# Kernel optimization log

Hardware: AMD Instinct MI355X
Metric: run time of the kernel (lower is better)

The kernel has to match this reference:

```python
import jax, jax.numpy as jnp
import numpy as np

EDGE_DIM = 64
NODE_DIM = 128
N_EDGES = 1_600_000
N_NODES = 50_000
LN_EPS = 1e-5


def setup_inputs() -> dict:
    key = jax.random.key(0)
    k1, k2, k3, k4 = jax.random.split(key, 4)
    edge_attr = jax.random.normal(k1, (N_EDGES, EDGE_DIM), dtype=jnp.float32)
    edge_index = jax.random.randint(k2, (2, N_EDGES), 0, N_NODES, dtype=jnp.int64)
    # Linear(edge_feat_dim, node_feat_dim) params (Kaiming-uniform-ish init)
    bound = 1.0 / np.sqrt(EDGE_DIM)
    W = jax.random.uniform(k3, (EDGE_DIM, NODE_DIM), dtype=jnp.float32, minval=-bound, maxval=bound)
    b = jax.random.uniform(k4, (NODE_DIM,), dtype=jnp.float32, minval=-bound, maxval=bound)
    gamma = jnp.ones((NODE_DIM,), dtype=jnp.float32)
    beta = jnp.zeros((NODE_DIM,), dtype=jnp.float32)
    return {"edge_attr": edge_attr, "W": W, "b": b, "gamma": gamma, "beta": beta,
            "edge_index": edge_index, "num_nodes": N_NODES}


def reference(edge_attr, W, b, gamma, beta, edge_index, num_nodes):
    # Edge transform: Linear -> ReLU -> LayerNorm
    h = jax.nn.relu(edge_attr @ W + b)  # [E, node_dim]
    mu = jnp.mean(h, axis=-1, keepdims=True)
    var = jnp.mean((h - mu) ** 2, axis=-1, keepdims=True)
    h = (h - mu) * jax.lax.rsqrt(var + LN_EPS) * gamma + beta
    src, dst = edge_index[0], edge_index[1]
    # Dual-endpoint scatter-add of transformed edge features
    node_features = (jax.ops.segment_sum(h, dst, num_segments=num_nodes)
                     + jax.ops.segment_sum(h, src, num_segments=num_nodes))  # [N, node_dim]
    ones = jnp.ones(src.shape[0], dtype=h.dtype)
    degree = (jax.ops.segment_sum(ones, src, num_segments=num_nodes)
              + jax.ops.segment_sum(ones, dst, num_segments=num_nodes))  # [N]
    degree = jnp.clip(degree, 1.0)[:, None]
    return node_features / degree
```

## Files before the change

### kernel.cpp

```cpp
#include <hip/hip_runtime.h>

constexpr int ED = 64;
constexpr int ND = 128;

__global__ __launch_bounds__(256)
void edge_scatter_kernel(const float* __restrict__ x,
                         const float* __restrict__ W,
                         const float* __restrict__ bias,
                         const float* __restrict__ gamma,
                         const float* __restrict__ beta,
                         const int*   __restrict__ ei,
                         int E,
                         float* __restrict__ out,
                         float* __restrict__ deg)
{
    __shared__ float4 Wq[32 * 64];

    for (int t = threadIdx.x; t < 32 * 64; t += 256) {
        const int k2 = t >> 6, j = t & 63;
        const float* Wr = W + (size_t)(2 * k2) * ND;
        Wq[t] = make_float4(Wr[j], Wr[64 + j], Wr[ND + j], Wr[ND + 64 + j]);
    }
    __syncthreads();

    const int lane = threadIdx.x & 63;
    const int wid  = blockIdx.x * (blockDim.x >> 6) + (threadIdx.x >> 6);
    const int nw   = gridDim.x * (blockDim.x >> 6);

    const float b0 = bias[lane],  b1 = bias[lane + 64];
    const float g0 = gamma[lane], g1 = gamma[lane + 64];
    const float p0 = beta[lane],  p1 = beta[lane + 64];

    const int ngroups = E >> 2;
    const int4* x4 = (const int4*)x;

    for (int g = wid; g < ngroups; g += nw) {
        const int e0 = g << 2;

        const int4 xi = x4[(size_t)g * 64 + lane];

        float h00 = b0, h01 = b1, h10 = b0, h11 = b1;
        float h20 = b0, h21 = b1, h30 = b0, h31 = b1;

#pragma unroll
        for (int kq = 0; kq < 16; ++kq) {
            const float4 wA = Wq[(2 * kq) * 64 + lane];
            const float4 wB = Wq[(2 * kq + 1) * 64 + lane];

            {
                const int ls = 0 * 16 + kq;
                const float a0 = __int_as_float(__builtin_amdgcn_readlane(xi.x, ls));
                const float a1 = __int_as_float(__builtin_amdgcn_readlane(xi.y, ls));
                const float a2 = __int_as_float(__builtin_amdgcn_readlane(xi.z, ls));
                const float a3 = __int_as_float(__builtin_amdgcn_readlane(xi.w, ls));
                h00 = fmaf(a0, wA.x, h00); h01 = fmaf(a0, wA.y, h01);
                h00 = fmaf(a1, wA.z, h00); h01 = fmaf(a1, wA.w, h01);
                h00 = fmaf(a2, wB.x, h00); h01 = fmaf(a2, wB.y, h01);
                h00 = fmaf(a3, wB.z, h00); h01 = fmaf(a3, wB.w, h01);
            }
            {
                const int ls = 1 * 16 + kq;
                const float a0 = __int_as_float(__builtin_amdgcn_readlane(xi.x, ls));
                const float a1 = __int_as_float(__builtin_amdgcn_readlane(xi.y, ls));
                const float a2 = __int_as_float(__builtin_amdgcn_readlane(xi.z, ls));
                const float a3 = __int_as_float(__builtin_amdgcn_readlane(xi.w, ls));
                h10 = fmaf(a0, wA.x, h10); h11 = fmaf(a0, wA.y, h11);
                h10 = fmaf(a1, wA.z, h10); h11 = fmaf(a1, wA.w, h11);
                h10 = fmaf(a2, wB.x, h10); h11 = fmaf(a2, wB.y, h11);
                h10 = fmaf(a3, wB.z, h10); h11 = fmaf(a3, wB.w, h11);
            }
            {
                const int ls = 2 * 16 + kq;
                const float a0 = __int_as_float(__builtin_amdgcn_readlane(xi.x, ls));
                const float a1 = __int_as_float(__builtin_amdgcn_readlane(xi.y, ls));
                const float a2 = __int_as_float(__builtin_amdgcn_readlane(xi.z, ls));
                const float a3 = __int_as_float(__builtin_amdgcn_readlane(xi.w, ls));
                h20 = fmaf(a0, wA.x, h20); h21 = fmaf(a0, wA.y, h21);
                h20 = fmaf(a1, wA.z, h20); h21 = fmaf(a1, wA.w, h21);
                h20 = fmaf(a2, wB.x, h20); h21 = fmaf(a2, wB.y, h21);
                h20 = fmaf(a3, wB.z, h20); h21 = fmaf(a3, wB.w, h21);
            }
            {
                const int ls = 3 * 16 + kq;
                const float a0 = __int_as_float(__builtin_amdgcn_readlane(xi.x, ls));
                const float a1 = __int_as_float(__builtin_amdgcn_readlane(xi.y, ls));
                const float a2 = __int_as_float(__builtin_amdgcn_readlane(xi.z, ls));
                const float a3 = __int_as_float(__builtin_amdgcn_readlane(xi.w, ls));
                h30 = fmaf(a0, wA.x, h30); h31 = fmaf(a0, wA.y, h31);
                h30 = fmaf(a1, wA.z, h30); h31 = fmaf(a1, wA.w, h31);
                h30 = fmaf(a2, wB.x, h30); h31 = fmaf(a2, wB.y, h31);
                h30 = fmaf(a3, wB.z, h30); h31 = fmaf(a3, wB.w, h31);
            }
        }

        h00 = fmaxf(h00, 0.f); h01 = fmaxf(h01, 0.f);
        h10 = fmaxf(h10, 0.f); h11 = fmaxf(h11, 0.f);
        h20 = fmaxf(h20, 0.f); h21 = fmaxf(h21, 0.f);
        h30 = fmaxf(h30, 0.f); h31 = fmaxf(h31, 0.f);

        float s0 = h00 + h01, q0 = fmaf(h00, h00, h01 * h01);
        float s1 = h10 + h11, q1 = fmaf(h10, h10, h11 * h11);
        float s2 = h20 + h21, q2 = fmaf(h20, h20, h21 * h21);
        float s3 = h30 + h31, q3 = fmaf(h30, h30, h31 * h31);
#pragma unroll
        for (int m = 1; m < 64; m <<= 1) {
            s0 += __shfl_xor(s0, m, 64); q0 += __shfl_xor(q0, m, 64);
            s1 += __shfl_xor(s1, m, 64); q1 += __shfl_xor(q1, m, 64);
            s2 += __shfl_xor(s2, m, 64); q2 += __shfl_xor(q2, m, 64);
            s3 += __shfl_xor(s3, m, 64); q3 += __shfl_xor(q3, m, 64);
        }
        const float inv = 1.0f / ND;
        const float mu0 = s0 * inv, rs0 = rsqrtf(q0 * inv - mu0 * mu0 + 1e-5f);
        const float mu1 = s1 * inv, rs1 = rsqrtf(q1 * inv - mu1 * mu1 + 1e-5f);
        const float mu2 = s2 * inv, rs2 = rsqrtf(q2 * inv - mu2 * mu2 + 1e-5f);
        const float mu3 = s3 * inv, rs3 = rsqrtf(q3 * inv - mu3 * mu3 + 1e-5f);

        const float y00 = (h00 - mu0) * rs0 * g0 + p0, y01 = (h01 - mu0) * rs0 * g1 + p1;
        const float y10 = (h10 - mu1) * rs1 * g0 + p0, y11 = (h11 - mu1) * rs1 * g1 + p1;
        const float y20 = (h20 - mu2) * rs2 * g0 + p0, y21 = (h21 - mu2) * rs2 * g1 + p1;
        const float y30 = (h30 - mu3) * rs3 * g0 + p0, y31 = (h31 - mu3) * rs3 * g1 + p1;

        const int sn0 = ei[e0 + 0], dn0 = ei[E + e0 + 0];
        const int sn1 = ei[e0 + 1], dn1 = ei[E + e0 + 1];
        const int sn2 = ei[e0 + 2], dn2 = ei[E + e0 + 2];
        const int sn3 = ei[e0 + 3], dn3 = ei[E + e0 + 3];

        unsafeAtomicAdd(&out[(size_t)dn0 * ND + lane],      y00);
        unsafeAtomicAdd(&out[(size_t)dn0 * ND + 64 + lane], y01);
        unsafeAtomicAdd(&out[(size_t)sn0 * ND + lane],      y00);
        unsafeAtomicAdd(&out[(size_t)sn0 * ND + 64 + lane], y01);
        unsafeAtomicAdd(&out[(size_t)dn1 * ND + lane],      y10);
        unsafeAtomicAdd(&out[(size_t)dn1 * ND + 64 + lane], y11);
        unsafeAtomicAdd(&out[(size_t)sn1 * ND + lane],      y10);
        unsafeAtomicAdd(&out[(size_t)sn1 * ND + 64 + lane], y11);
        unsafeAtomicAdd(&out[(size_t)dn2 * ND + lane],      y20);
        unsafeAtomicAdd(&out[(size_t)dn2 * ND + 64 + lane], y21);
        unsafeAtomicAdd(&out[(size_t)sn2 * ND + lane],      y20);
        unsafeAtomicAdd(&out[(size_t)sn2 * ND + 64 + lane], y21);
        unsafeAtomicAdd(&out[(size_t)dn3 * ND + lane],      y30);
        unsafeAtomicAdd(&out[(size_t)dn3 * ND + 64 + lane], y31);
        unsafeAtomicAdd(&out[(size_t)sn3 * ND + lane],      y30);
        unsafeAtomicAdd(&out[(size_t)sn3 * ND + 64 + lane], y31);

        int nid = dn0;
        if (lane == 1) nid = dn1;
        if (lane == 2) nid = dn2;
        if (lane == 3) nid = dn3;
        if (lane == 4) nid = sn0;
        if (lane == 5) nid = sn1;
        if (lane == 6) nid = sn2;
        if (lane == 7) nid = sn3;
        if (lane < 8) unsafeAtomicAdd(&deg[nid], 1.0f);
    }

    for (int e = (ngroups << 2) + wid; e < E; e += nw) {
        const int xv = __float_as_int(x[(size_t)e * ED + lane]);
        float h0 = b0, h1 = b1;
#pragma unroll
        for (int kq = 0; kq < 16; ++kq) {
            const float4 wA = Wq[(2 * kq) * 64 + lane];
            const float4 wB = Wq[(2 * kq + 1) * 64 + lane];
            const float a0 = __int_as_float(__builtin_amdgcn_readlane(xv, 4 * kq + 0));
            const float a1 = __int_as_float(__builtin_amdgcn_readlane(xv, 4 * kq + 1));
            const float a2 = __int_as_float(__builtin_amdgcn_readlane(xv, 4 * kq + 2));
            const float a3 = __int_as_float(__builtin_amdgcn_readlane(xv, 4 * kq + 3));
            h0 = fmaf(a0, wA.x, h0); h1 = fmaf(a0, wA.y, h1);
            h0 = fmaf(a1, wA.z, h0); h1 = fmaf(a1, wA.w, h1);
            h0 = fmaf(a2, wB.x, h0); h1 = fmaf(a2, wB.y, h1);
            h0 = fmaf(a3, wB.z, h0); h1 = fmaf(a3, wB.w, h1);
        }
        h0 = fmaxf(h0, 0.f); h1 = fmaxf(h1, 0.f);
        float s = h0 + h1, q = fmaf(h0, h0, h1 * h1);
#pragma unroll
        for (int m = 1; m < 64; m <<= 1) {
            s += __shfl_xor(s, m, 64); q += __shfl_xor(q, m, 64);
        }
        const float mu = s / ND, rs = rsqrtf(q / ND - mu * mu + 1e-5f);
        const float y0 = (h0 - mu) * rs * g0 + p0, y1 = (h1 - mu) * rs * g1 + p1;
        const int sn = ei[e], dn = ei[E + e];
        unsafeAtomicAdd(&out[(size_t)dn * ND + lane],      y0);
        unsafeAtomicAdd(&out[(size_t)dn * ND + 64 + lane], y1);
        unsafeAtomicAdd(&out[(size_t)sn * ND + lane],      y0);
        unsafeAtomicAdd(&out[(size_t)sn * ND + 64 + lane], y1);
        if (lane == 0) unsafeAtomicAdd(&deg[dn], 1.0f);
        if (lane == 1) unsafeAtomicAdd(&deg[sn], 1.0f);
    }
}

__global__ void finalize_kernel(float4* __restrict__ out,
                                const float* __restrict__ deg,
                                int n4)
{
    const int i = blockIdx.x * blockDim.x + threadIdx.x;
    if (i < n4) {
        const float d = fmaxf(deg[i >> 5], 1.0f);
        float4 v = out[i];
        v.x /= d; v.y /= d; v.z /= d; v.w /= d;
        out[i] = v;
    }
}

extern "C" void kernel_launch(void* const* d_in, const int* in_sizes, int n_in,
                              void* d_out, int out_size, void* d_ws, size_t ws_size,
                              hipStream_t stream)
{
    const float* x     = (const float*)d_in[0];
    const float* W     = (const float*)d_in[1];
    const float* bias  = (const float*)d_in[2];
    const float* gamma = (const float*)d_in[3];
    const float* beta  = (const float*)d_in[4];
    const int*   ei    = (const int*)d_in[5];

    const int E       = in_sizes[0] / ED;
    const int n_nodes = out_size / ND;

    float* out = (float*)d_out;
    float* deg = (float*)d_ws;

    hipMemsetAsync(d_out, 0, (size_t)out_size * sizeof(float), stream);
    hipMemsetAsync(d_ws,  0, (size_t)n_nodes * sizeof(float), stream);

    edge_scatter_kernel<<<4096, 256, 0, stream>>>(x, W, bias, gamma, beta,
                                                  ei, E, out, deg);

    finalize_kernel<<<(out_size / 4 + 255) / 256, 256, 0, stream>>>(
        (float4*)out, deg, out_size / 4);
}
```

Measured before the change: 1.898 ms.

## Replace atomic scatter-add with CSR build and per-node gather

Splits the fused kernel into stages. First, compute the LayerNorm-ed edge features into a workspace buffer while counting node degrees. Then prefix-scan the counts, fill a node-to-edge adjacency list, and have one wavefront per node gather and average its incident edge rows. This removes the per-element float atomics on the output, at the cost of a large intermediate write and read plus a single-block scan. It also adds nontemporal loads and stores. It falls back to the old atomic path when the workspace is too small.

```diff
diff --git a/kernel.cpp b/kernel.cpp
--- a/kernel.cpp
+++ b/kernel.cpp
@@ -2,6 +2,275 @@
 
 constexpr int ED = 64;
 constexpr int ND = 128;
+
+typedef int   iv4 __attribute__((ext_vector_type(4)));
+typedef float fv2 __attribute__((ext_vector_type(2)));
+
+__global__ __launch_bounds__(256)
+void transform_kernel(const float* __restrict__ x,
+                      const float* __restrict__ W,
+                      const float* __restrict__ bias,
+                      const float* __restrict__ gamma,
+                      const float* __restrict__ beta,
+                      const int*   __restrict__ ei,
+                      int E,
+                      float* __restrict__ h,
+                      unsigned* __restrict__ cnt)
+{
+    __shared__ float4 Wq[32 * 64];
+
+    for (int t = threadIdx.x; t < 32 * 64; t += 256) {
+        const int k2 = t >> 6, j = t & 63;
+        const float* Wr = W + (size_t)(2 * k2) * ND;
+        Wq[t] = make_float4(Wr[j], Wr[64 + j], Wr[ND + j], Wr[ND + 64 + j]);
+    }
+    __syncthreads();
+
+    const int lane = threadIdx.x & 63;
+    const int wid  = blockIdx.x * (blockDim.x >> 6) + (threadIdx.x >> 6);
+    const int nw   = gridDim.x * (blockDim.x >> 6);
+
+    const float b0 = bias[lane],  b1 = bias[lane + 64];
+    const float g0 = gamma[lane], g1 = gamma[lane + 64];
+    const float p0 = beta[lane],  p1 = beta[lane + 64];
+
+    const int ngroups = E >> 2;
+    const iv4* x4 = (const iv4*)x;
+
+    for (int g = wid; g < ngroups; g += nw) {
+        const int e0 = g << 2;
+        const iv4 xi = __builtin_nontemporal_load(&x4[(size_t)g * 64 + lane]);
+
+        const int sn0 = ei[e0 + 0], dn0 = ei[E + e0 + 0];
+        const int sn1 = ei[e0 + 1], dn1 = ei[E + e0 + 1];
+        const int sn2 = ei[e0 + 2], dn2 = ei[E + e0 + 2];
+        const int sn3 = ei[e0 + 3], dn3 = ei[E + e0 + 3];
+
+        float h00 = b0, h01 = b1, h10 = b0, h11 = b1;
+        float h20 = b0, h21 = b1, h30 = b0, h31 = b1;
+
+#pragma unroll
+        for (int kq = 0; kq < 16; ++kq) {
+            const float4 wA = Wq[(2 * kq) * 64 + lane];
+            const float4 wB = Wq[(2 * kq + 1) * 64 + lane];
+            {
+                const int ls = 0 * 16 + kq;
+                const float a0 = __int_as_float(__builtin_amdgcn_readlane(xi.x, ls));
+                const float a1 = __int_as_float(__builtin_amdgcn_readlane(xi.y, ls));
+                const float a2 = __int_as_float(__builtin_amdgcn_readlane(xi.z, ls));
+                const float a3 = __int_as_float(__builtin_amdgcn_readlane(xi.w, ls));
+                h00 = fmaf(a0, wA.x, h00); h01 = fmaf(a0, wA.y, h01);
+                h00 = fmaf(a1, wA.z, h00); h01 = fmaf(a1, wA.w, h01);
+                h00 = fmaf(a2, wB.x, h00); h01 = fmaf(a2, wB.y, h01);
+                h00 = fmaf(a3, wB.z, h00); h01 = fmaf(a3, wB.w, h01);
+            }
+            {
+                const int ls = 1 * 16 + kq;
+                const float a0 = __int_as_float(__builtin_amdgcn_readlane(xi.x, ls));
+                const float a1 = __int_as_float(__builtin_amdgcn_readlane(xi.y, ls));
+                const float a2 = __int_as_float(__builtin_amdgcn_readlane(xi.z, ls));
+                const float a3 = __int_as_float(__builtin_amdgcn_readlane(xi.w, ls));
+                h10 = fmaf(a0, wA.x, h10); h11 = fmaf(a0, wA.y, h11);
+                h10 = fmaf(a1, wA.z, h10); h11 = fmaf(a1, wA.w, h11);
+                h10 = fmaf(a2, wB.x, h10); h11 = fmaf(a2, wB.y, h11);
+                h10 = fmaf(a3, wB.z, h10); h11 = fmaf(a3, wB.w, h11);
+            }
+            {
+                const int ls = 2 * 16 + kq;
+                const float a0 = __int_as_float(__builtin_amdgcn_readlane(xi.x, ls));
+                const float a1 = __int_as_float(__builtin_amdgcn_readlane(xi.y, ls));
+                const float a2 = __int_as_float(__builtin_amdgcn_readlane(xi.z, ls));
+                const float a3 = __int_as_float(__builtin_amdgcn_readlane(xi.w, ls));
+                h20 = fmaf(a0, wA.x, h20); h21 = fmaf(a0, wA.y, h21);
+                h20 = fmaf(a1, wA.z, h20); h21 = fmaf(a1, wA.w, h21);
+                h20 = fmaf(a2, wB.x, h20); h21 = fmaf(a2, wB.y, h21);
+                h20 = fmaf(a3, wB.z, h20); h21 = fmaf(a3, wB.w, h21);
+            }
+            {
+                const int ls = 3 * 16 + kq;
+                const float a0 = __int_as_float(__builtin_amdgcn_readlane(xi.x, ls));
+                const float a1 = __int_as_float(__builtin_amdgcn_readlane(xi.y, ls));
+                const float a2 = __int_as_float(__builtin_amdgcn_readlane(xi.z, ls));
+                const float a3 = __int_as_float(__builtin_amdgcn_readlane(xi.w, ls));
+                h30 = fmaf(a0, wA.x, h30); h31 = fmaf(a0, wA.y, h31);
+                h30 = fmaf(a1, wA.z, h30); h31 = fmaf(a1, wA.w, h31);
+                h30 = fmaf(a2, wB.x, h30); h31 = fmaf(a2, wB.y, h31);
+                h30 = fmaf(a3, wB.z, h30); h31 = fmaf(a3, wB.w, h31);
+            }
+        }
+
+        h00 = fmaxf(h00, 0.f); h01 = fmaxf(h01, 0.f);
+        h10 = fmaxf(h10, 0.f); h11 = fmaxf(h11, 0.f);
+        h20 = fmaxf(h20, 0.f); h21 = fmaxf(h21, 0.f);
+        h30 = fmaxf(h30, 0.f); h31 = fmaxf(h31, 0.f);
+
+        float s0 = h00 + h01, q0 = fmaf(h00, h00, h01 * h01);
+        float s1 = h10 + h11, q1 = fmaf(h10, h10, h11 * h11);
+        float s2 = h20 + h21, q2 = fmaf(h20, h20, h21 * h21);
+        float s3 = h30 + h31, q3 = fmaf(h30, h30, h31 * h31);
+#pragma unroll
+        for (int m = 1; m < 64; m <<= 1) {
+            s0 += __shfl_xor(s0, m, 64); q0 += __shfl_xor(q0, m, 64);
+            s1 += __shfl_xor(s1, m, 64); q1 += __shfl_xor(q1, m, 64);
+            s2 += __shfl_xor(s2, m, 64); q2 += __shfl_xor(q2, m, 64);
+            s3 += __shfl_xor(s3, m, 64); q3 += __shfl_xor(q3, m, 64);
+        }
+        const float inv = 1.0f / ND;
+        const float mu0 = s0 * inv, rs0 = rsqrtf(q0 * inv - mu0 * mu0 + 1e-5f);
+        const float mu1 = s1 * inv, rs1 = rsqrtf(q1 * inv - mu1 * mu1 + 1e-5f);
+        const float mu2 = s2 * inv, rs2 = rsqrtf(q2 * inv - mu2 * mu2 + 1e-5f);
+        const float mu3 = s3 * inv, rs3 = rsqrtf(q3 * inv - mu3 * mu3 + 1e-5f);
+
+        const float y00 = (h00 - mu0) * rs0 * g0 + p0, y01 = (h01 - mu0) * rs0 * g1 + p1;
+        const float y10 = (h10 - mu1) * rs1 * g0 + p0, y11 = (h11 - mu1) * rs1 * g1 + p1;
+        const float y20 = (h20 - mu2) * rs2 * g0 + p0, y21 = (h21 - mu2) * rs2 * g1 + p1;
+        const float y30 = (h30 - mu3) * rs3 * g0 + p0, y31 = (h31 - mu3) * rs3 * g1 + p1;
+
+        float* hr0 = h + (size_t)(e0 + 0) * ND;
+        float* hr1 = h + (size_t)(e0 + 1) * ND;
+        float* hr2 = h + (size_t)(e0 + 2) * ND;
+        float* hr3 = h + (size_t)(e0 + 3) * ND;
+        __builtin_nontemporal_store(y00, hr0 + lane);
+        __builtin_nontemporal_store(y01, hr0 + 64 + lane);
+        __builtin_nontemporal_store(y10, hr1 + lane);
+        __builtin_nontemporal_store(y11, hr1 + 64 + lane);
+        __builtin_nontemporal_store(y20, hr2 + lane);
+        __builtin_nontemporal_store(y21, hr2 + 64 + lane);
+        __builtin_nontemporal_store(y30, hr3 + lane);
+        __builtin_nontemporal_store(y31, hr3 + 64 + lane);
+
+        int nid = dn0;
+        if (lane == 1) nid = dn1;
+        if (lane == 2) nid = dn2;
+        if (lane == 3) nid = dn3;
+        if (lane == 4) nid = sn0;
+        if (lane == 5) nid = sn1;
+        if (lane == 6) nid = sn2;
+        if (lane == 7) nid = sn3;
+        if (lane < 8) atomicAdd(&cnt[nid], 1u);
+    }
+
+    for (int e = (ngroups << 2) + wid; e < E; e += nw) {
+        const int xv = __float_as_int(x[(size_t)e * ED + lane]);
+        float h0 = b0, h1 = b1;
+#pragma unroll
+        for (int kq = 0; kq < 16; ++kq) {
+            const float4 wA = Wq[(2 * kq) * 64 + lane];
+            const float4 wB = Wq[(2 * kq + 1) * 64 + lane];
+            const float a0 = __int_as_float(__builtin_amdgcn_readlane(xv, 4 * kq + 0));
+            const float a1 = __int_as_float(__builtin_amdgcn_readlane(xv, 4 * kq + 1));
+            const float a2 = __int_as_float(__builtin_amdgcn_readlane(xv, 4 * kq + 2));
+            const float a3 = __int_as_float(__builtin_amdgcn_readlane(xv, 4 * kq + 3));
+            h0 = fmaf(a0, wA.x, h0); h1 = fmaf(a0, wA.y, h1);
+            h0 = fmaf(a1, wA.z, h0); h1 = fmaf(a1, wA.w, h1);
+            h0 = fmaf(a2, wB.x, h0); h1 = fmaf(a2, wB.y, h1);
+            h0 = fmaf(a3, wB.z, h0); h1 = fmaf(a3, wB.w, h1);
+        }
+        h0 = fmaxf(h0, 0.f); h1 = fmaxf(h1, 0.f);
+        float s = h0 + h1, q = fmaf(h0, h0, h1 * h1);
+#pragma unroll
+        for (int m = 1; m < 64; m <<= 1) {
+            s += __shfl_xor(s, m, 64); q += __shfl_xor(q, m, 64);
+        }
+        const float mu = s / ND, rs = rsqrtf(q / ND - mu * mu + 1e-5f);
+        const float y0 = (h0 - mu) * rs * g0 + p0, y1 = (h1 - mu) * rs * g1 + p1;
+        float* hr = h + (size_t)e * ND;
+        __builtin_nontemporal_store(y0, hr + lane);
+        __builtin_nontemporal_store(y1, hr + 64 + lane);
+        const int sn = ei[e], dn = ei[E + e];
+        if (lane == 0) atomicAdd(&cnt[dn], 1u);
+        if (lane == 1) atomicAdd(&cnt[sn], 1u);
+    }
+}
+
+__global__ __launch_bounds__(1024)
+void scan_kernel(const unsigned* __restrict__ cnt,
+                 unsigned* __restrict__ offs,
+                 int N)
+{
+    __shared__ unsigned part[1024];
+    const int t = threadIdx.x;
+    const int chunk = (N + 1023) / 1024;
+    const int lo = t * chunk;
+    const int hi = (lo + chunk < N) ? lo + chunk : N;
+
+    unsigned s = 0;
+    for (int i = lo; i < hi; ++i) s += cnt[i];
+    part[t] = s;
+    __syncthreads();
+
+    for (int d = 1; d < 1024; d <<= 1) {
+        unsigned v = (t >= d) ? part[t - d] : 0u;
+        __syncthreads();
+        part[t] += v;
+        __syncthreads();
+    }
+
+    unsigned run = (t == 0) ? 0u : part[t - 1];
+    for (int i = lo; i < hi; ++i) { offs[i] = run; run += cnt[i]; }
+    if (t == 0) offs[N] = part[1023];
+}
+
+__global__ __launch_bounds__(256)
+void fill_kernel(const int* __restrict__ ei,
+                 int E,
+                 const unsigned* __restrict__ offs,
+                 unsigned* __restrict__ cursor,
+                 int* __restrict__ adj)
+{
+    const int E2 = 2 * E;
+    for (int i = blockIdx.x * blockDim.x + threadIdx.x; i < E2;
+         i += gridDim.x * blockDim.x) {
+        const int n = ei[i];
+        const unsigned pos = offs[n] + atomicAdd(&cursor[n], 1u);
+        adj[pos] = (i < E) ? i : i - E;
+    }
+}
+
+__global__ __launch_bounds__(256)
+void gather_kernel(const float* __restrict__ h,
+                   const unsigned* __restrict__ offs,
+                   const int* __restrict__ adj,
+                   float* __restrict__ out,
+                   int N)
+{
+    const int lane = threadIdx.x & 63;
+    const int w = blockIdx.x * (blockDim.x >> 6) + (threadIdx.x >> 6);
+    if (w >= N) return;
+
+    const unsigned o0 = offs[w], o1 = offs[w + 1];
+    const fv2* h2 = (const fv2*)h;
+
+    float a0 = 0.f, a1 = 0.f;
+    for (unsigned base = o0; base < o1; base += 64) {
+        const int m = (int)((o1 - base < 64u) ? (o1 - base) : 64u);
+        int av = 0;
+        if (base + (unsigned)lane < o1) av = adj[base + lane];
+
+        int j = 0;
+        for (; j + 4 <= m; j += 4) {
+            const int e0 = __builtin_amdgcn_readlane(av, j + 0);
+            const int e1 = __builtin_amdgcn_readlane(av, j + 1);
+            const int e2 = __builtin_amdgcn_readlane(av, j + 2);
+            const int e3 = __builtin_amdgcn_readlane(av, j + 3);
+            const fv2 v0 = h2[(size_t)e0 * 64 + lane];
+            const fv2 v1 = h2[(size_t)e1 * 64 + lane];
+            const fv2 v2 = h2[(size_t)e2 * 64 + lane];
+            const fv2 v3 = h2[(size_t)e3 * 64 + lane];
+            a0 += v0.x + v1.x + v2.x + v3.x;
+            a1 += v0.y + v1.y + v2.y + v3.y;
+        }
+        for (; j < m; ++j) {
+            const int e = __builtin_amdgcn_readlane(av, j);
+            const fv2 v = h2[(size_t)e * 64 + lane];
+            a0 += v.x; a1 += v.y;
+        }
+    }
+
+    const float inv = 1.0f / fmaxf((float)(o1 - o0), 1.0f);
+    fv2 r; r.x = a0 * inv; r.y = a1 * inv;
+    ((fv2*)out)[(size_t)w * 64 + lane] = r;
+}
 
 __global__ __launch_bounds__(256)
 void edge_scatter_kernel(const float* __restrict__ x,
@@ -15,7 +284,6 @@
                          float* __restrict__ deg)
 {
     __shared__ float4 Wq[32 * 64];
-
     for (int t = threadIdx.x; t < 32 * 64; t += 256) {
         const int k2 = t >> 6, j = t & 63;
         const float* Wr = W + (size_t)(2 * k2) * ND;
@@ -32,12 +300,11 @@
     const float p0 = beta[lane],  p1 = beta[lane + 64];
 
     const int ngroups = E >> 2;
-    const int4* x4 = (const int4*)x;
+    const iv4* x4 = (const iv4*)x;
 
     for (int g = wid; g < ngroups; g += nw) {
         const int e0 = g << 2;
-
-        const int4 xi = x4[(size_t)g * 64 + lane];
+        const iv4 xi = __builtin_nontemporal_load(&x4[(size_t)g * 64 + lane]);
 
         float h00 = b0, h01 = b1, h10 = b0, h11 = b1;
         float h20 = b0, h21 = b1, h30 = b0, h31 = b1;
@@ -46,7 +313,6 @@
         for (int kq = 0; kq < 16; ++kq) {
             const float4 wA = Wq[(2 * kq) * 64 + lane];
             const float4 wB = Wq[(2 * kq + 1) * 64 + lane];
-
             {
                 const int ls = 0 * 16 + kq;
                 const float a0 = __int_as_float(__builtin_amdgcn_readlane(xi.x, ls));
@@ -200,6 +466,8 @@
     }
 }
 
+static inline size_t align_up(size_t v, size_t a) { return (v + a - 1) & ~(a - 1); }
+
 extern "C" void kernel_launch(void* const* d_in, const int* in_sizes, int n_in,
                               void* d_out, int out_size, void* d_ws, size_t ws_size,
                               hipStream_t stream)
@@ -211,18 +479,41 @@
     const float* beta  = (const float*)d_in[4];
     const int*   ei    = (const int*)d_in[5];
 
-    const int E       = in_sizes[0] / ED;
-    const int n_nodes = out_size / ND;
-
-    float* out = (float*)d_out;
-    float* deg = (float*)d_ws;
-
-    hipMemsetAsync(d_out, 0, (size_t)out_size * sizeof(float), stream);
-    hipMemsetAsync(d_ws,  0, (size_t)n_nodes * sizeof(float), stream);
-
-    edge_scatter_kernel<<<4096, 256, 0, stream>>>(x, W, bias, gamma, beta,
-                                                  ei, E, out, deg);
-
-    finalize_kernel<<<(out_size / 4 + 255) / 256, 256, 0, stream>>>(
-        (float4*)out, deg, out_size / 4);
-}
+    const int E = in_sizes[0] / ED;
+    const int N = out_size / ND;
+
+    const size_t off_h    = 0;
+    const size_t off_offs = align_up(off_h + (size_t)E * ND * sizeof(float), 16);
+    const size_t off_cnt  = align_up(off_offs + ((size_t)N + 1) * 4, 16);
+    const size_t off_cur  = align_up(off_cnt + (size_t)N * 4, 16);
+    const size_t off_adj  = align_up(off_cur + (size_t)N * 4, 16);
+    const size_t need     = off_adj + (size_t)2 * E * 4;
+
+    if (ws_size >= need) {
+        char* ws = (char*)d_ws;
+        float*    h      = (float*)(ws + off_h);
+        unsigned* offs   = (unsigned*)(ws + off_offs);
+        unsigned* cnt    = (unsigned*)(ws + off_cnt);
+        unsigned* cursor = (unsigned*)(ws + off_cur);
+        int*      adj    = (int*)(ws + off_adj);
+        float*    out    = (float*)d_out;
+
+        (void)hipMemsetAsync(cnt,    0, (size_t)N * 4, stream);
+        (void)hipMemsetAsync(cursor, 0, (size_t)N * 4, stream);
+
+        transform_kernel<<<4096, 256, 0, stream>>>(x, W, bias, gamma, beta,
+                                                   ei, E, h, cnt);
+        scan_kernel<<<1, 1024, 0, stream>>>(cnt, offs, N);
+        fill_kernel<<<2048, 256, 0, stream>>>(ei, E, offs, cursor, adj);
+        gather_kernel<<<(N + 3) / 4, 256, 0, stream>>>(h, offs, adj, out, N);
+    } else {
+        float* out = (float*)d_out;
+        float* deg = (float*)d_ws;
+        (void)hipMemsetAsync(d_out, 0, (size_t)out_size * sizeof(float), stream);
+        (void)hipMemsetAsync(d_ws,  0, (size_t)N * sizeof(float), stream);
+        edge_scatter_kernel<<<4096, 256, 0, stream>>>(x, W, bias, gamma, beta,
+                                                      ei, E, out, deg);
+        finalize_kernel<<<(out_size / 4 + 255) / 256, 256, 0, stream>>>(
+            (float4*)out, deg, out_size / 4);
+    }
+}
```

After: 1.821 ms. -4.1%, faster.
